# Kernel tuning notes

Hardware: AMD Instinct MI355X
Metric: run time of the kernel (lower is better)

The kernel has to match this reference:

```python
import jax, jax.numpy as jnp
import numpy as np

D_MODEL, D_K, D_V, N_HEADS = 1024, 64, 64, 16
B, S = 2, 2048
LN_EPS = 1e-5


def setup_inputs() -> dict:
    key = jax.random.key(0)
    ks = jax.random.split(key, 12)
    s = 1.0 / np.sqrt(D_MODEL)
    inp = {
        "Q": jax.random.normal(ks[0], (B, S, D_MODEL), jnp.float32),
        "K": jax.random.normal(ks[1], (B, S, D_MODEL), jnp.float32),
        "V": jax.random.normal(ks[2], (B, S, D_MODEL), jnp.float32),
        "attn_mask": jax.random.bernoulli(ks[3], 0.1, (B, S, S)),
        "Wq": jax.random.uniform(ks[4], (D_MODEL, D_K * N_HEADS), jnp.float32, -s, s),
        "bq": jnp.zeros((D_K * N_HEADS,), jnp.float32),
        "Wk": jax.random.uniform(ks[5], (D_MODEL, D_K * N_HEADS), jnp.float32, -s, s),
        "bk": jnp.zeros((D_K * N_HEADS,), jnp.float32),
        "Wv": jax.random.uniform(ks[6], (D_MODEL, D_V * N_HEADS), jnp.float32, -s, s),
        "bv": jnp.zeros((D_V * N_HEADS,), jnp.float32),
        "Wo": jax.random.uniform(ks[7], (N_HEADS * D_V, D_MODEL), jnp.float32, -s, s),
        "bo": jnp.zeros((D_MODEL,), jnp.float32),
        "gamma": jnp.ones((D_MODEL,), jnp.float32),
        "beta": jnp.zeros((D_MODEL,), jnp.float32),
    }
    return inp


def reference(Q, K, V, attn_mask, Wq, bq, Wk, bk, Wv, bv, Wo, bo, gamma, beta):
    b, s, _ = Q.shape
    # projections -> [B, S, H, d]
    q = (Q @ Wq + bq).reshape(b, s, N_HEADS, D_K)
    k = (K @ Wk + bk).reshape(b, -1, N_HEADS, D_K)
    v = (V @ Wv + bv).reshape(b, -1, N_HEADS, D_V)
    # scores [B, H, Sq, Sk]
    scores = jnp.einsum("bqhd,bkhd->bhqk", q, k) / np.sqrt(D_K).astype(np.float32)
    scores = jnp.where(attn_mask[:, None, :, :], jnp.float32(-1e9), scores)
    attn = jax.nn.softmax(scores, axis=-1)
    context = jnp.einsum("bhqk,bkhd->bqhd", attn, v).reshape(b, s, N_HEADS * D_V)
    out = context @ Wo + bo + Q  # residual
    mu = jnp.mean(out, axis=-1, keepdims=True)
    var = jnp.var(out, axis=-1, keepdims=True)
    return (out - mu) * jax.lax.rsqrt(var + LN_EPS) * gamma + beta
```

## Files before the change

kernel.cpp:

```cpp
#include <hip/hip_runtime.h>
#include <hip/hip_bf16.h>
#include <math.h>


#define D_MODEL 1024
#define NHEADS  16
#define DHEAD   64
#define BATCH   2
#define SEQ     2048
#define MROWS   (BATCH * SEQ)
#define SCLF    0.18033688f

typedef __attribute__((ext_vector_type(8)))  short bf16x8;
typedef __attribute__((ext_vector_type(4)))  float f32x4;
typedef __attribute__((ext_vector_type(16))) float f32x16;

__device__ inline unsigned short f2bf(float f) {
    unsigned int u = __builtin_bit_cast(unsigned int, f);
    unsigned int r = (u + 0x7FFFu + ((u >> 16) & 1u)) >> 16;
    return (unsigned short)r;
}

__device__ inline unsigned cvtpk_bf16(float lo, float hi2) {
    unsigned r;
    asm("v_cvt_pk_bf16_f32 %0, %1, %2" : "=v"(r) : "v"(lo), "v"(hi2));
    return r;
}

__device__ inline void gload16(const unsigned short* g, unsigned short* lbase, int lane) {
#if __has_builtin(__builtin_amdgcn_global_load_lds)
    __builtin_amdgcn_global_load_lds(
        (const __attribute__((address_space(1))) unsigned int*)g,
        (__attribute__((address_space(3))) unsigned int*)lbase, 16, 0, 0);
#else
    *(bf16x8*)(lbase + lane * 8) = *(const bf16x8*)g;
#endif
}

__global__ __launch_bounds__(256) void detect_mask_par(
    const unsigned int* __restrict__ m, int nwords, int* __restrict__ flags)
{
    const int i = blockIdx.x * 256 + threadIdx.x;
    int a = 0, b = 0;
    if (i < nwords) {
        const unsigned int w = m[i];
        a = (w != 0u && w != 1u);
        b = (w != 0u && w != 0x3F800000u);
    }
    const int wa = (int)__any(a);
    const int wb = (int)__any(b);
    if ((threadIdx.x & 63) == 0) {
        if (wa) atomicOr(&flags[0], 1);
        if (wb) atomicOr(&flags[1], 1);
    }
}

__global__ __launch_bounds__(256) void pack_mask_ballot(
    const void* __restrict__ mask, const int* __restrict__ flags,
    unsigned long long* __restrict__ mbits, int nwords)
{
    const int lane   = threadIdx.x & 63;
    const int wv     = blockIdx.x * 4 + (threadIdx.x >> 6);
    const int nwaves = gridDim.x * 4;
    const int mf = (flags[0] == 0) ? 0 : (flags[1] == 0) ? 1 : 2;
    for (int w = wv; w < nwords; w += nwaves) {
        bool bit;
        if (mf == 0)      bit = ((const unsigned int*)mask)[(size_t)w * 64 + lane] != 0u;
        else if (mf == 1) bit = ((const float*)mask)[(size_t)w * 64 + lane] != 0.f;
        else              bit = ((const unsigned char*)mask)[(size_t)w * 64 + lane] != 0;
        const unsigned long long b = __ballot(bit);
        if (lane == 0) mbits[w] = b;
    }
}

__global__ __launch_bounds__(256) void cvt_bf16(
    const float* __restrict__ s0, const float* __restrict__ s1,
    const float* __restrict__ s2,
    unsigned short* __restrict__ d0, unsigned short* __restrict__ d1,
    unsigned short* __restrict__ d2)
{
    const float* s = (blockIdx.y == 0) ? s0 : (blockIdx.y == 1) ? s1 : s2;
    unsigned short* d = (blockIdx.y == 0) ? d0 : (blockIdx.y == 1) ? d1 : d2;
    const int i = blockIdx.x * 256 + threadIdx.x;
    float4 a = ((const float4*)s)[i * 2];
    float4 b = ((const float4*)s)[i * 2 + 1];
    unsigned u0 = cvtpk_bf16(a.x, a.y);
    unsigned u1 = cvtpk_bf16(a.z, a.w);
    unsigned u2 = cvtpk_bf16(b.x, b.y);
    unsigned u3 = cvtpk_bf16(b.z, b.w);
    ((int4*)d)[i] = make_int4((int)u0, (int)u1, (int)u2, (int)u3);
}

__global__ __launch_bounds__(256) void cvt_wT(
    const float* __restrict__ w0, const float* __restrict__ w1,
    const float* __restrict__ w2, const float* __restrict__ w3,
    unsigned short* __restrict__ t0, unsigned short* __restrict__ t1,
    unsigned short* __restrict__ t2, unsigned short* __restrict__ t3)
{
    __shared__ float tile[64][65];
    const float* W = (blockIdx.z == 0) ? w0 : (blockIdx.z == 1) ? w1
                   : (blockIdx.z == 2) ? w2 : w3;
    unsigned short* T = (blockIdx.z == 0) ? t0 : (blockIdx.z == 1) ? t1
                      : (blockIdx.z == 2) ? t2 : t3;
    const int k0 = blockIdx.y * 64;
    const int n0 = blockIdx.x * 64;
    const int t  = threadIdx.x;
    const int r  = t >> 4;
    const int c4 = (t & 15) * 4;
    #pragma unroll
    for (int u = 0; u < 4; ++u) {
        float4 v = *(const float4*)(W + (size_t)(k0 + r + u * 16) * D_MODEL + n0 + c4);
        tile[r + u * 16][c4 + 0] = v.x;
        tile[r + u * 16][c4 + 1] = v.y;
        tile[r + u * 16][c4 + 2] = v.z;
        tile[r + u * 16][c4 + 3] = v.w;
    }
    __syncthreads();
    #pragma unroll
    for (int u = 0; u < 4; ++u) {
        const int nr = r + u * 16;
        ushort4 o;
        o.x = f2bf(tile[c4 + 0][nr]);
        o.y = f2bf(tile[c4 + 1][nr]);
        o.z = f2bf(tile[c4 + 2][nr]);
        o.w = f2bf(tile[c4 + 3][nr]);
        *(ushort4*)(T + (size_t)(n0 + nr) * D_MODEL + k0 + c4) = o;
    }
}

#define BKK 64

__global__ __launch_bounds__(256, 1) void gemm_qkv(
    const unsigned short* __restrict__ A0, const unsigned short* __restrict__ A1,
    const unsigned short* __restrict__ A2,
    const unsigned short* __restrict__ B0, const unsigned short* __restrict__ B1,
    const unsigned short* __restrict__ B2,
    const float* __restrict__ bias0, const float* __restrict__ bias1,
    const float* __restrict__ bias2,
    unsigned short* __restrict__ C0, unsigned short* __restrict__ C1,
    unsigned short* __restrict__ C2)
{
    const int z = blockIdx.z;
    const unsigned short* A  = (z == 0) ? A0 : (z == 1) ? A1 : A2;
    const unsigned short* Bt = (z == 0) ? B0 : (z == 1) ? B1 : B2;
    const float* bias        = (z == 0) ? bias0 : (z == 1) ? bias1 : bias2;
    unsigned short* C        = (z == 0) ? C0 : (z == 1) ? C1 : C2;
    const int K = D_MODEL, N = D_MODEL;

    __shared__ unsigned short As[2][128 * BKK];
    __shared__ unsigned short Bs[2][128 * BKK];
    const int tid  = threadIdx.x;
    const int w    = tid >> 6;
    const int lane = tid & 63;
    const int lo   = lane & 15;
    const int hi   = lane >> 4;
    const int wm   = (w >> 1) * 64;
    const int wn   = (w & 1) * 64;
    const int m0   = blockIdx.x * 128;
    const int n0   = blockIdx.y * 128;

    const unsigned short* Ab = A  + (size_t)m0 * K;
    const unsigned short* Bb = Bt + (size_t)n0 * K;

    f32x4 acc[4][4];
    #pragma unroll
    for (int i = 0; i < 4; ++i)
        #pragma unroll
        for (int j = 0; j < 4; ++j) acc[i][j] = (f32x4){0.f, 0.f, 0.f, 0.f};

    const int NT = K / BKK;
    auto stage = [&](int buf, int t) {
        const int k0 = t * BKK;
        #pragma unroll
        for (int i = 0; i < 4; ++i) {
            const int c = i * 256 + tid;
            gload16(Ab + (size_t)(c >> 3) * K + k0 + (c & 7) * 8,
                    &As[buf][(i * 256 + w * 64) * 8], lane);
        }
        #pragma unroll
        for (int i = 0; i < 4; ++i) {
            const int c = i * 256 + tid;
            gload16(Bb + (size_t)(c >> 3) * K + k0 + (c & 7) * 8,
                    &Bs[buf][(i * 256 + w * 64) * 8], lane);
        }
    };

    stage(0, 0);
    __syncthreads();
    int cur = 0;
    for (int t = 0; t < NT; ++t) {
        if (t + 1 < NT) stage(cur ^ 1, t + 1);
        bf16x8 af[4][2], bfr[4][2];
        #pragma unroll
        for (int f = 0; f < 4; ++f)
            #pragma unroll
            for (int s = 0; s < 2; ++s) {
                af[f][s]  = *(const bf16x8*)&As[cur][(wm + f * 16 + lo) * BKK + s * 32 + hi * 8];
                bfr[f][s] = *(const bf16x8*)&Bs[cur][(wn + f * 16 + lo) * BKK + s * 32 + hi * 8];
            }
        #pragma unroll
        for (int s = 0; s < 2; ++s)
            #pragma unroll
            for (int fm = 0; fm < 4; ++fm)
                #pragma unroll
                for (int fn = 0; fn < 4; ++fn)
                    acc[fm][fn] = __builtin_amdgcn_mfma_f32_16x16x32_bf16(
                        af[fm][s], bfr[fn][s], acc[fm][fn], 0, 0, 0);
        __syncthreads();
        cur ^= 1;
    }

    #pragma unroll
    for (int fm = 0; fm < 4; ++fm) {
        const int row = m0 + wm + fm * 16 + hi * 4;
        #pragma unroll
        for (int fn = 0; fn < 4; ++fn) {
            const int col = n0 + wn + fn * 16 + lo;
            const float bv = bias[col];
            #pragma unroll
            for (int r = 0; r < 4; ++r) {
                float o = acc[fm][fn][r] + bv;
                if (z == 0) o *= SCLF;
                if (z < 2)
                    C[(size_t)(row + r) * N + col] = f2bf(o);
                else
                    C[(size_t)((row + r) >> 11) * 2097152
                      + (size_t)col * 2048 + ((row + r) & 2047)] = f2bf(o);
            }
        }
    }
}

__global__ __launch_bounds__(256) void gemm_out64(
    const unsigned short* __restrict__ A, const unsigned short* __restrict__ Bt,
    const float* __restrict__ bias, const float* __restrict__ resid,
    float* __restrict__ C)
{
    const int K = D_MODEL, N = D_MODEL;
    __shared__ unsigned short As[2][128 * BKK];
    __shared__ unsigned short Bs[2][64 * BKK];
    const int tid  = threadIdx.x;
    const int w    = tid >> 6;
    const int lane = tid & 63;
    const int lo   = lane & 15;
    const int hi   = lane >> 4;
    const int wm   = (w >> 1) * 64;
    const int wn   = (w & 1) * 32;
    const int m0   = blockIdx.x * 128;
    const int n0   = blockIdx.y * 64;

    const unsigned short* Ab = A  + (size_t)m0 * K;
    const unsigned short* Bb = Bt + (size_t)n0 * K;

    f32x4 acc[4][2];
    #pragma unroll
    for (int i = 0; i < 4; ++i)
        #pragma unroll
        for (int j = 0; j < 2; ++j) acc[i][j] = (f32x4){0.f, 0.f, 0.f, 0.f};

    const int NT = K / BKK;
    auto stage = [&](int buf, int t) {
        const int k0 = t * BKK;
        #pragma unroll
        for (int i = 0; i < 4; ++i) {
            const int c = i * 256 + tid;
            gload16(Ab + (size_t)(c >> 3) * K + k0 + (c & 7) * 8,
                    &As[buf][(i * 256 + w * 64) * 8], lane);
        }
        #pragma unroll
        for (int i = 0; i < 2; ++i) {
            const int c = i * 256 + tid;
            gload16(Bb + (size_t)(c >> 3) * K + k0 + (c & 7) * 8,
                    &Bs[buf][(i * 256 + w * 64) * 8], lane);
        }
    };

    stage(0, 0);
    __syncthreads();
    int cur = 0;
    for (int t = 0; t < NT; ++t) {
        if (t + 1 < NT) stage(cur ^ 1, t + 1);
        bf16x8 af[4][2], bfr[2][2];
        #pragma unroll
        for (int f = 0; f < 4; ++f)
            #pragma unroll
            for (int s = 0; s < 2; ++s)
                af[f][s] = *(const bf16x8*)&As[cur][(wm + f * 16 + lo) * BKK + s * 32 + hi * 8];
        #pragma unroll
        for (int f = 0; f < 2; ++f)
            #pragma unroll
            for (int s = 0; s < 2; ++s)
                bfr[f][s] = *(const bf16x8*)&Bs[cur][(wn + f * 16 + lo) * BKK + s * 32 + hi * 8];
        #pragma unroll
        for (int s = 0; s < 2; ++s)
            #pragma unroll
            for (int fm = 0; fm < 4; ++fm)
                #pragma unroll
                for (int fn = 0; fn < 2; ++fn)
                    acc[fm][fn] = __builtin_amdgcn_mfma_f32_16x16x32_bf16(
                        af[fm][s], bfr[fn][s], acc[fm][fn], 0, 0, 0);
        __syncthreads();
        cur ^= 1;
    }

    #pragma unroll
    for (int fm = 0; fm < 4; ++fm) {
        const int row = m0 + wm + fm * 16 + hi * 4;
        #pragma unroll
        for (int fn = 0; fn < 2; ++fn) {
            const int col = n0 + wn + fn * 16 + lo;
            const float bv = bias[col];
            #pragma unroll
            for (int r = 0; r < 4; ++r)
                C[(size_t)(row + r) * N + col] =
                    acc[fm][fn][r] + bv + resid[(size_t)(row + r) * N + col];
        }
    }
}

__global__ __launch_bounds__(512, 2) void attn_mfma32(
    const unsigned short* __restrict__ qb, const unsigned short* __restrict__ kbm,
    const unsigned short* __restrict__ vt,
    const unsigned long long* __restrict__ mbits, unsigned short* __restrict__ ctx)
{
    __shared__ unsigned char smem[65536];
    const int tid  = threadIdx.x;
    const int w8   = tid >> 6;
    const int g    = w8 >> 2;
    const int wq   = w8 & 3;
    const int lane = tid & 63;
    const int l31  = lane & 31;
    const int hi   = lane >> 5;
    const int h    = blockIdx.x;
    const int q0   = blockIdx.y * 128;
    const int b    = blockIdx.z;

    unsigned short* KsG = (unsigned short*)smem + (size_t)g * 8192;
    unsigned short* VsG = (unsigned short*)(smem + 32768) + (size_t)g * 8192;

    const size_t qkbase = (size_t)b * SEQ * D_MODEL + (size_t)h * DHEAD;
    const size_t vtbase = ((size_t)b * D_MODEL + h * DHEAD) * SEQ;

    const int qtok = q0 + wq * 32 + l31;
    bf16x8 qA[4];
    #pragma unroll
    for (int s = 0; s < 4; ++s)
        qA[s] = *(const bf16x8*)(qb + qkbase + (size_t)qtok * D_MODEL + s * 16 + hi * 8);

    f32x16 o0 = {}, o1 = {};
    float l_i = 0.f;

    const unsigned long long* mrow = mbits + ((size_t)b * SEQ + qtok) * (SEQ / 64);

    const int srow = lane >> 3;
    const int sc   = lane & 7;
    const int r0   = wq * 16 + srow;
    const int swz  = sc ^ (r0 & 7);

    const unsigned short* kl0 = kbm + qkbase + (size_t)(g * 1024 + r0) * D_MODEL + swz * 8;
    const unsigned short* kl1 = kl0 + (size_t)8 * D_MODEL;
    const unsigned short* vl0 = vt + vtbase + (size_t)r0 * SEQ + g * 1024 + swz * 8;
    const unsigned short* vl1 = vl0 + (size_t)8 * SEQ;
    const int ldk0 = (wq * 16) * 64;
    const int ldk1 = (wq * 16 + 8) * 64;

    auto stage = [&](int buf) {
        gload16(kl0, &KsG[buf * 4096 + ldk0], lane);
        gload16(kl1, &KsG[buf * 4096 + ldk1], lane);
        gload16(vl0, &VsG[buf * 4096 + ldk0], lane);
        gload16(vl1, &VsG[buf * 4096 + ldk1], lane);
        kl0 += (size_t)64 * D_MODEL;
        kl1 += (size_t)64 * D_MODEL;
        vl0 += 64;
        vl1 += 64;
    };

    stage(0);
    unsigned long long mw64 = mrow[g * 16];
    __syncthreads();
    int cur = 0;

    for (int t = 0; t < 16; ++t) {
        if (t + 1 < 16) stage(cur ^ 1);
        const unsigned long long mwc = mw64;
        if (t + 1 < 16) mw64 = mrow[g * 16 + t + 1];
        const unsigned int ml = (unsigned int)(mwc >> (4 * hi));
        const unsigned int mh = (unsigned int)(mwc >> (32 + 4 * hi));

        f32x16 st0 = {}, st1 = {};
        __builtin_amdgcn_s_setprio(1);
        #pragma unroll
        for (int s = 0; s < 4; ++s) {
            bf16x8 kf0 = *(const bf16x8*)&KsG[cur * 4096 + l31 * 64 + ((2 * s + hi) ^ (l31 & 7)) * 8];
            st0 = __builtin_amdgcn_mfma_f32_32x32x16_bf16(kf0, qA[s], st0, 0, 0, 0);
            bf16x8 kf1 = *(const bf16x8*)&KsG[cur * 4096 + (32 + l31) * 64 + ((2 * s + hi) ^ (l31 & 7)) * 8];
            st1 = __builtin_amdgcn_mfma_f32_32x32x16_bf16(kf1, qA[s], st1, 0, 0, 0);
        }
        __builtin_amdgcn_s_setprio(0);

        float sp[4] = {0.f, 0.f, 0.f, 0.f};
        #pragma unroll
        for (int r = 0; r < 16; ++r) {
            const int klo = (r & 3) + 8 * (r >> 2);
            const float x0 = ((ml >> klo) & 1u) ? -1e9f : st0[r];
            const float x1 = ((mh >> klo) & 1u) ? -1e9f : st1[r];
            const float e0 = exp2f(x0);
            const float e1 = exp2f(x1);
            st0[r] = e0; st1[r] = e1;
            sp[r & 3] += e0 + e1;
        }
        l_i += (sp[0] + sp[1]) + (sp[2] + sp[3]);

        bf16x8 pa[4];
        #pragma unroll
        for (int s = 0; s < 4; ++s) {
            const int base = (s & 1) * 8;
            unsigned av, bv2, cv, dv;
            if (s < 2) {
                av  = cvtpk_bf16(st0[base + 0], st0[base + 1]);
                bv2 = cvtpk_bf16(st0[base + 4], st0[base + 5]);
                cv  = cvtpk_bf16(st0[base + 2], st0[base + 3]);
                dv  = cvtpk_bf16(st0[base + 6], st0[base + 7]);
            } else {
                av  = cvtpk_bf16(st1[base + 0], st1[base + 1]);
                bv2 = cvtpk_bf16(st1[base + 4], st1[base + 5]);
                cv  = cvtpk_bf16(st1[base + 2], st1[base + 3]);
                dv  = cvtpk_bf16(st1[base + 6], st1[base + 7]);
            }
            asm("v_permlane32_swap_b32 %0, %1" : "+v"(av), "+v"(bv2));
            asm("v_permlane32_swap_b32 %0, %1" : "+v"(cv), "+v"(dv));
            int4 pk = make_int4((int)av, (int)cv, (int)bv2, (int)dv);
            pa[s] = __builtin_bit_cast(bf16x8, pk);
        }

        __builtin_amdgcn_s_setprio(1);
        #pragma unroll
        for (int s = 0; s < 4; ++s) {
            bf16x8 vf0 = *(const bf16x8*)&VsG[cur * 4096 + l31 * 64 + ((2 * s + hi) ^ (l31 & 7)) * 8];
            o0 = __builtin_amdgcn_mfma_f32_32x32x16_bf16(pa[s], vf0, o0, 0, 0, 0);
            bf16x8 vf1 = *(const bf16x8*)&VsG[cur * 4096 + (32 + l31) * 64 + ((2 * s + hi) ^ (l31 & 7)) * 8];
            o1 = __builtin_amdgcn_mfma_f32_32x32x16_bf16(pa[s], vf1, o1, 0, 0, 0);
        }
        __builtin_amdgcn_s_setprio(0);
        __syncthreads();
        cur ^= 1;
    }

    l_i += __shfl_xor(l_i, 32, 64);
    __syncthreads();
    float* comb = (float*)smem;
    if (g == 1) {
        float* p = comb + (size_t)(wq * 64 + lane) * 33;
        #pragma unroll
        for (int r = 0; r < 16; ++r) { p[r] = o0[r]; p[16 + r] = o1[r]; }
        p[32] = l_i;
    }
    __syncthreads();
    if (g == 0) {
        const float* p = comb + (size_t)(wq * 64 + lane) * 33;
        const float inv = 1.f / (l_i + p[32]);
        #pragma unroll
        for (int r = 0; r < 16; ++r) {
            const int qloc = (r & 3) + 8 * (r >> 2) + 4 * hi;
            const float ivr = __shfl(inv, qloc, 64);
            unsigned short* dst = ctx + qkbase + (size_t)(q0 + wq * 32 + qloc) * D_MODEL;
            dst[l31]      = f2bf((o0[r] + p[r]) * ivr);
            dst[32 + l31] = f2bf((o1[r] + p[16 + r]) * ivr);
        }
    }
}

__global__ __launch_bounds__(256) void layernorm1024(
    const float* __restrict__ x, const float* __restrict__ gamma,
    const float* __restrict__ beta, float* __restrict__ out)
{
    const int row = blockIdx.x;
    const int tid = threadIdx.x;
    const float* xr = x + (size_t)row * D_MODEL;
    float4 v = *(const float4*)(xr + (tid << 2));
    float s = v.x + v.y + v.z + v.w;
    float q = v.x * v.x + v.y * v.y + v.z * v.z + v.w * v.w;
    #pragma unroll
    for (int off = 1; off < 64; off <<= 1) {
        s += __shfl_xor(s, off, 64);
        q += __shfl_xor(q, off, 64);
    }
    __shared__ float sw[4], qw_[4];
    const int wid = tid >> 6;
    if ((tid & 63) == 0) { sw[wid] = s; qw_[wid] = q; }
    __syncthreads();
    s = sw[0] + sw[1] + sw[2] + sw[3];
    q = qw_[0] + qw_[1] + qw_[2] + qw_[3];
    const float mu  = s * (1.f / D_MODEL);
    const float var = q * (1.f / D_MODEL) - mu * mu;
    const float a = var + 1e-5f;
    float inv = rsqrtf(a);
    inv = inv * (1.5f - 0.5f * a * inv * inv);
    float4 gg = *(const float4*)(gamma + (tid << 2));
    float4 bt = *(const float4*)(beta + (tid << 2));
    float4 o;
    o.x = (v.x - mu) * inv * gg.x + bt.x;
    o.y = (v.y - mu) * inv * gg.y + bt.y;
    o.z = (v.z - mu) * inv * gg.z + bt.z;
    o.w = (v.w - mu) * inv * gg.w + bt.w;
    *(float4*)(out + (size_t)row * D_MODEL + (tid << 2)) = o;
}

extern "C" void kernel_launch(void* const* d_in, const int* in_sizes, int n_in,
                              void* d_out, int out_size, void* d_ws, size_t ws_size,
                              hipStream_t stream)
{
    const float* Q    = (const float*)d_in[0];
    const float* K    = (const float*)d_in[1];
    const float* V    = (const float*)d_in[2];
    const void*  mask = d_in[3];
    const float* Wq   = (const float*)d_in[4];
    const float* bq   = (const float*)d_in[5];
    const float* Wk   = (const float*)d_in[6];
    const float* bk   = (const float*)d_in[7];
    const float* Wv   = (const float*)d_in[8];
    const float* bv   = (const float*)d_in[9];
    const float* Wo   = (const float*)d_in[10];
    const float* bo   = (const float*)d_in[11];
    const float* gam  = (const float*)d_in[12];
    const float* bet  = (const float*)d_in[13];
    float* out = (float*)d_out;

    const size_t NE = (size_t)MROWS * D_MODEL;
    const size_t WE = (size_t)D_MODEL * D_MODEL;
    const size_t NMW = (size_t)BATCH * SEQ * (SEQ / 64);
    unsigned short* Qbf = (unsigned short*)d_ws;
    unsigned short* Kbf = Qbf + NE;
    unsigned short* Vbf = Kbf + NE;
    unsigned short* qb  = Vbf + NE;
    unsigned short* kb  = qb + NE;
    unsigned short* vt  = kb + NE;
    unsigned short* Wt0 = vt + NE;
    unsigned short* Wt1 = Wt0 + WE;
    unsigned short* Wt2 = Wt1 + WE;
    unsigned short* Wt3 = Wt2 + WE;
    unsigned long long* mbits = (unsigned long long*)(Wt3 + WE);
    int* mflags = (int*)(mbits + NMW);
    unsigned short* ctxb = Qbf;
    float* outp = (float*)Kbf;
    if (ws_size < 6 * NE * 2 + 4 * WE * 2 + NMW * 8 + 64) return;

    hipMemsetAsync(mflags, 0, 2 * sizeof(int), stream);
    detect_mask_par<<<256, 256, 0, stream>>>((const unsigned int*)mask, 65536, mflags);
    pack_mask_ballot<<<2048, 256, 0, stream>>>(mask, mflags, mbits, (int)NMW);

    cvt_bf16<<<dim3(NE / 8 / 256, 3), 256, 0, stream>>>(Q, K, V, Qbf, Kbf, Vbf);
    cvt_wT<<<dim3(16, 16, 4), 256, 0, stream>>>(Wq, Wk, Wv, Wo, Wt0, Wt1, Wt2, Wt3);

    gemm_qkv<<<dim3(32, 8, 3), 256, 0, stream>>>(Qbf, Kbf, Vbf, Wt0, Wt1, Wt2,
                                                 bq, bk, bv, qb, kb, vt);

    dim3 ag(NHEADS, SEQ / 128, BATCH);
    attn_mfma32<<<ag, 512, 0, stream>>>(qb, kb, vt, mbits, ctxb);

    gemm_out64<<<dim3(32, 16), 256, 0, stream>>>(ctxb, Wt3, bo, Q, outp);

    layernorm1024<<<MROWS, 256, 0, stream>>>(outp, gam, bet, out);
}
```

Measured before the change: 218.2 us.

## Merge conversion kernels into one launch and shrink QKV GEMM K-tile to 32

Merges the activation bf16 conversion and the weight transpose-convert into a single cvt_all launch, with blockIdx.z choosing the job, which saves one kernel launch. Surplus blocks on the weight planes exit early. Separately, gemm_qkv's K-tile drops from 64 to 32, halving its LDS footprint and fragment registers. This may allow more resident blocks, but it doubles the number of barrier-synchronised iterations and cuts the MFMA work done per sync.

After: 187.3 us. 1.17x faster.

```diff
diff --git a/kernel.cpp b/kernel.cpp
--- a/kernel.cpp
+++ b/kernel.cpp
@@ -73,63 +73,62 @@
     }
 }
 
-__global__ __launch_bounds__(256) void cvt_bf16(
-    const float* __restrict__ s0, const float* __restrict__ s1,
-    const float* __restrict__ s2,
-    unsigned short* __restrict__ d0, unsigned short* __restrict__ d1,
-    unsigned short* __restrict__ d2)
-{
-    const float* s = (blockIdx.y == 0) ? s0 : (blockIdx.y == 1) ? s1 : s2;
-    unsigned short* d = (blockIdx.y == 0) ? d0 : (blockIdx.y == 1) ? d1 : d2;
-    const int i = blockIdx.x * 256 + threadIdx.x;
-    float4 a = ((const float4*)s)[i * 2];
-    float4 b = ((const float4*)s)[i * 2 + 1];
-    unsigned u0 = cvtpk_bf16(a.x, a.y);
-    unsigned u1 = cvtpk_bf16(a.z, a.w);
-    unsigned u2 = cvtpk_bf16(b.x, b.y);
-    unsigned u3 = cvtpk_bf16(b.z, b.w);
-    ((int4*)d)[i] = make_int4((int)u0, (int)u1, (int)u2, (int)u3);
-}
-
-__global__ __launch_bounds__(256) void cvt_wT(
+__global__ __launch_bounds__(256) void cvt_all(
+    const float* __restrict__ Q, const float* __restrict__ K,
+    const float* __restrict__ V,
     const float* __restrict__ w0, const float* __restrict__ w1,
     const float* __restrict__ w2, const float* __restrict__ w3,
+    unsigned short* __restrict__ Qb, unsigned short* __restrict__ Kb,
+    unsigned short* __restrict__ Vb,
     unsigned short* __restrict__ t0, unsigned short* __restrict__ t1,
     unsigned short* __restrict__ t2, unsigned short* __restrict__ t3)
 {
     __shared__ float tile[64][65];
-    const float* W = (blockIdx.z == 0) ? w0 : (blockIdx.z == 1) ? w1
-                   : (blockIdx.z == 2) ? w2 : w3;
-    unsigned short* T = (blockIdx.z == 0) ? t0 : (blockIdx.z == 1) ? t1
-                      : (blockIdx.z == 2) ? t2 : t3;
-    const int k0 = blockIdx.y * 64;
-    const int n0 = blockIdx.x * 64;
-    const int t  = threadIdx.x;
-    const int r  = t >> 4;
-    const int c4 = (t & 15) * 4;
-    #pragma unroll
-    for (int u = 0; u < 4; ++u) {
-        float4 v = *(const float4*)(W + (size_t)(k0 + r + u * 16) * D_MODEL + n0 + c4);
-        tile[r + u * 16][c4 + 0] = v.x;
-        tile[r + u * 16][c4 + 1] = v.y;
-        tile[r + u * 16][c4 + 2] = v.z;
-        tile[r + u * 16][c4 + 3] = v.w;
-    }
-    __syncthreads();
-    #pragma unroll
-    for (int u = 0; u < 4; ++u) {
-        const int nr = r + u * 16;
-        ushort4 o;
-        o.x = f2bf(tile[c4 + 0][nr]);
-        o.y = f2bf(tile[c4 + 1][nr]);
-        o.z = f2bf(tile[c4 + 2][nr]);
-        o.w = f2bf(tile[c4 + 3][nr]);
-        *(ushort4*)(T + (size_t)(n0 + nr) * D_MODEL + k0 + c4) = o;
-    }
-}
-
-#define BKK 64
-
+    const int z = blockIdx.z;
+    if (z < 3) {
+        const float* s = (z == 0) ? Q : (z == 1) ? K : V;
+        unsigned short* d = (z == 0) ? Qb : (z == 1) ? Kb : Vb;
+        const int i = blockIdx.x * 256 + threadIdx.x;
+        float4 a = ((const float4*)s)[i * 2];
+        float4 b = ((const float4*)s)[i * 2 + 1];
+        unsigned u0 = cvtpk_bf16(a.x, a.y);
+        unsigned u1 = cvtpk_bf16(a.z, a.w);
+        unsigned u2 = cvtpk_bf16(b.x, b.y);
+        unsigned u3 = cvtpk_bf16(b.z, b.w);
+        ((int4*)d)[i] = make_int4((int)u0, (int)u1, (int)u2, (int)u3);
+    } else {
+        if (blockIdx.x >= 256) return;
+        const int wz = z - 3;
+        const float* W = (wz == 0) ? w0 : (wz == 1) ? w1 : (wz == 2) ? w2 : w3;
+        unsigned short* T = (wz == 0) ? t0 : (wz == 1) ? t1 : (wz == 2) ? t2 : t3;
+        const int n0 = (blockIdx.x & 15) * 64;
+        const int k0 = (blockIdx.x >> 4) * 64;
+        const int t  = threadIdx.x;
+        const int r  = t >> 4;
+        const int c4 = (t & 15) * 4;
+        #pragma unroll
+        for (int u = 0; u < 4; ++u) {
+            float4 v = *(const float4*)(W + (size_t)(k0 + r + u * 16) * D_MODEL + n0 + c4);
+            tile[r + u * 16][c4 + 0] = v.x;
+            tile[r + u * 16][c4 + 1] = v.y;
+            tile[r + u * 16][c4 + 2] = v.z;
+            tile[r + u * 16][c4 + 3] = v.w;
+        }
+        __syncthreads();
+        #pragma unroll
+        for (int u = 0; u < 4; ++u) {
+            const int nr = r + u * 16;
+            ushort4 o;
+            o.x = f2bf(tile[c4 + 0][nr]);
+            o.y = f2bf(tile[c4 + 1][nr]);
+            o.z = f2bf(tile[c4 + 2][nr]);
+            o.w = f2bf(tile[c4 + 3][nr]);
+            *(ushort4*)(T + (size_t)(n0 + nr) * D_MODEL + k0 + c4) = o;
+        }
+    }
+}
+
+#define BKQ 32
 __global__ __launch_bounds__(256, 1) void gemm_qkv(
     const unsigned short* __restrict__ A0, const unsigned short* __restrict__ A1,
     const unsigned short* __restrict__ A2,
@@ -147,8 +146,8 @@
     unsigned short* C        = (z == 0) ? C0 : (z == 1) ? C1 : C2;
     const int K = D_MODEL, N = D_MODEL;
 
-    __shared__ unsigned short As[2][128 * BKK];
-    __shared__ unsigned short Bs[2][128 * BKK];
+    __shared__ unsigned short As[2][128 * BKQ];
+    __shared__ unsigned short Bs[2][128 * BKQ];
     const int tid  = threadIdx.x;
     const int w    = tid >> 6;
     const int lane = tid & 63;
@@ -168,19 +167,19 @@
         #pragma unroll
         for (int j = 0; j < 4; ++j) acc[i][j] = (f32x4){0.f, 0.f, 0.f, 0.f};
 
-    const int NT = K / BKK;
+    const int NT = K / BKQ;
     auto stage = [&](int buf, int t) {
-        const int k0 = t * BKK;
-        #pragma unroll
-        for (int i = 0; i < 4; ++i) {
+        const int k0 = t * BKQ;
+        #pragma unroll
+        for (int i = 0; i < 2; ++i) {
             const int c = i * 256 + tid;
-            gload16(Ab + (size_t)(c >> 3) * K + k0 + (c & 7) * 8,
+            gload16(Ab + (size_t)(c >> 2) * K + k0 + (c & 3) * 8,
                     &As[buf][(i * 256 + w * 64) * 8], lane);
         }
         #pragma unroll
-        for (int i = 0; i < 4; ++i) {
+        for (int i = 0; i < 2; ++i) {
             const int c = i * 256 + tid;
-            gload16(Bb + (size_t)(c >> 3) * K + k0 + (c & 7) * 8,
+            gload16(Bb + (size_t)(c >> 2) * K + k0 + (c & 3) * 8,
                     &Bs[buf][(i * 256 + w * 64) * 8], lane);
         }
     };
@@ -190,22 +189,18 @@
     int cur = 0;
     for (int t = 0; t < NT; ++t) {
         if (t + 1 < NT) stage(cur ^ 1, t + 1);
-        bf16x8 af[4][2], bfr[4][2];
-        #pragma unroll
-        for (int f = 0; f < 4; ++f)
+        bf16x8 af[4], bfr[4];
+        #pragma unroll
+        for (int f = 0; f < 4; ++f) {
+            af[f]  = *(const bf16x8*)&As[cur][(wm + f * 16 + lo) * BKQ + hi * 8];
+            bfr[f] = *(const bf16x8*)&Bs[cur][(wn + f * 16 + lo) * BKQ + hi * 8];
+        }
+        #pragma unroll
+        for (int fm = 0; fm < 4; ++fm)
             #pragma unroll
-            for (int s = 0; s < 2; ++s) {
-                af[f][s]  = *(const bf16x8*)&As[cur][(wm + f * 16 + lo) * BKK + s * 32 + hi * 8];
-                bfr[f][s] = *(const bf16x8*)&Bs[cur][(wn + f * 16 + lo) * BKK + s * 32 + hi * 8];
-            }
-        #pragma unroll
-        for (int s = 0; s < 2; ++s)
-            #pragma unroll
-            for (int fm = 0; fm < 4; ++fm)
-                #pragma unroll
-                for (int fn = 0; fn < 4; ++fn)
-                    acc[fm][fn] = __builtin_amdgcn_mfma_f32_16x16x32_bf16(
-                        af[fm][s], bfr[fn][s], acc[fm][fn], 0, 0, 0);
+            for (int fn = 0; fn < 4; ++fn)
+                acc[fm][fn] = __builtin_amdgcn_mfma_f32_16x16x32_bf16(
+                    af[fm], bfr[fn], acc[fm][fn], 0, 0, 0);
         __syncthreads();
         cur ^= 1;
     }
@@ -231,6 +226,7 @@
     }
 }
 
+#define BKK 64
 __global__ __launch_bounds__(256) void gemm_out64(
     const unsigned short* __restrict__ A, const unsigned short* __restrict__ Bt,
     const float* __restrict__ bias, const float* __restrict__ resid,
@@ -549,8 +545,8 @@
     detect_mask_par<<<256, 256, 0, stream>>>((const unsigned int*)mask, 65536, mflags);
     pack_mask_ballot<<<2048, 256, 0, stream>>>(mask, mflags, mbits, (int)NMW);
 
-    cvt_bf16<<<dim3(NE / 8 / 256, 3), 256, 0, stream>>>(Q, K, V, Qbf, Kbf, Vbf);
-    cvt_wT<<<dim3(16, 16, 4), 256, 0, stream>>>(Wq, Wk, Wv, Wo, Wt0, Wt1, Wt2, Wt3);
+    cvt_all<<<dim3(2048, 1, 7), 256, 0, stream>>>(Q, K, V, Wq, Wk, Wv, Wo,
+                                                  Qbf, Kbf, Vbf, Wt0, Wt1, Wt2, Wt3);
 
     gemm_qkv<<<dim3(32, 8, 3), 256, 0, stream>>>(Qbf, Kbf, Vbf, Wt0, Wt1, Wt2,
                                                  bq, bk, bv, qb, kb, vt);
```
